# Optimization experiments

Hardware: AMD Instinct MI355X
Metric: run time of the kernel (lower is better)

Reference implementation:

```python
import jax, jax.numpy as jnp
import numpy as np

EPS = 1e-8

def _safe_norm(x):
    # L2 norm over last axis with zero (not NaN) gradient at x == 0,
    # matching torch.norm's subgradient convention.
    sq = jnp.sum(x * x, axis=-1, keepdims=True)
    nz = sq > 0
    return jnp.sqrt(jnp.where(nz, sq, 1.0)) * jnp.where(nz, 1.0, 0.0)

def _dihedral(p1, p2, p3, p4):
    # p*: [..., 3] -> angle [...], signed, in radians
    v1 = p2 - p1
    v2 = p3 - p2
    v3 = p4 - p3
    n1 = jnp.cross(v1, v2)
    n2 = jnp.cross(v2, v3)
    n1n = n1 / (_safe_norm(n1) + EPS)
    n2n = n2 / (_safe_norm(n2) + EPS)
    cos_angle = jnp.clip(jnp.sum(n1n * n2n, axis=-1), -1.0, 1.0)
    angle = jnp.arccos(cos_angle)
    sign = jnp.sign(jnp.sum(n1n * v3, axis=-1))
    return angle * sign

def setup_inputs() -> dict:
    key = jax.random.key(0)
    k1, k2, k3 = jax.random.split(key, 3)
    B, L, D = 64, 4096, 64
    backbone_coords = jax.random.normal(k1, (B, L, 4, 3), dtype=jnp.float32)
    # nn.Linear(6, 64): kaiming-uniform-ish init, bound = 1/sqrt(6)
    bound = 1.0 / np.sqrt(6.0)
    W = jax.random.uniform(k2, (D, 6), minval=-bound, maxval=bound, dtype=jnp.float32)
    b = jax.random.uniform(k3, (D,), minval=-bound, maxval=bound, dtype=jnp.float32)
    return {"backbone_coords": backbone_coords, "W": W, "b": b}

def reference(backbone_coords, W, b):
    # backbone_coords: [B, L, 4, 3] with atoms N, CA, C, O
    N = backbone_coords[:, :, 0, :]
    CA = backbone_coords[:, :, 1, :]
    C = backbone_coords[:, :, 2, :]

    # Shifted neighbors, duplicating boundary atoms exactly as the loop branches do.
    C_prev = jnp.concatenate([C[:, :1], C[:, :-1]], axis=1)      # phi i==0: p1 = C[0]
    N_next = jnp.concatenate([N[:, 1:], N[:, -1:]], axis=1)      # psi i==L-1: p4 = N[L-1]
    om_p3 = jnp.concatenate([N[:, 1:], CA[:, -1:]], axis=1)      # omega i==L-1: p3 = CA[L-1]
    om_p4 = jnp.concatenate([CA[:, 1:], CA[:, -1:]], axis=1)     # omega i==L-1: p4 = CA[L-1]

    phi = _dihedral(C_prev, N, CA, C)     # [B, L]
    psi = _dihedral(N, CA, C, N_next)     # [B, L]
    omega = _dihedral(CA, C, om_p3, om_p4)  # [B, L]

    angles = jnp.stack([phi, psi, omega], axis=-1)                     # [B, L, 3]
    encoded = jnp.concatenate([jnp.sin(angles), jnp.cos(angles)], axis=-1)  # [B, L, 6]
    return encoded @ W.T + b              # [B, L, 64]
```

## Files before the change

kernel.cpp:

```cpp
#include <hip/hip_runtime.h>

#define L_RES 4096
#define EPSF 1e-8f

struct V3 { float x, y, z; };

__device__ __forceinline__ V3 v3sub(V3 a, V3 b) { return {a.x-b.x, a.y-b.y, a.z-b.z}; }
__device__ __forceinline__ V3 v3cross(V3 a, V3 b) {
    return {a.y*b.z - a.z*b.y, a.z*b.x - a.x*b.z, a.x*b.y - a.y*b.x};
}
__device__ __forceinline__ float v3dot(V3 a, V3 b) { return a.x*b.x + a.y*b.y + a.z*b.z; }

__device__ __forceinline__ void dihedral_sc(V3 p1, V3 p2, V3 p3, V3 p4,
                                            float& s_out, float& c_out) {
    V3 v1 = v3sub(p2, p1);
    V3 v2 = v3sub(p3, p2);
    V3 v3 = v3sub(p4, p3);
    V3 n1 = v3cross(v1, v2);
    V3 n2 = v3cross(v2, v3);
    float sq1 = v3dot(n1, n1);
    float sq2 = v3dot(n2, n2);
    float nrm1 = (sq1 > 0.f) ? sqrtf(sq1) : 0.f;
    float nrm2 = (sq2 > 0.f) ? sqrtf(sq2) : 0.f;
    float inv1 = 1.f / (nrm1 + EPSF);
    float inv2 = 1.f / (nrm2 + EPSF);
    float c = (n1.x*n2.x + n1.y*n2.y + n1.z*n2.z) * (inv1 * inv2);
    c = fminf(1.f, fmaxf(-1.f, c));
    float sg = (n1.x*v3.x + n1.y*v3.y + n1.z*v3.z) * inv1;
    float sgn = (sg > 0.f) ? 1.f : ((sg < 0.f) ? -1.f : 0.f);
    float s = sqrtf(fmaxf(0.f, (1.f - c) * (1.f + c)));
    s_out = sgn * s;
    c_out = (sg == 0.f) ? 1.f : c;
}

__global__ __launch_bounds__(256) void dihedral_enc_kernel(
        const float* __restrict__ coords,
        const float* __restrict__ W,
        const float* __restrict__ bias,
        float* __restrict__ out) {
    __shared__ float enc_s[256 * 7];

    const int t   = threadIdx.x;
    const int blk = blockIdx.x;
    const int b   = blk >> 4;
    const int l   = ((blk & 15) << 8) + t;

    const long rowf = (long)b * L_RES * 12;
    const long ownf = rowf + (long)l * 12;
    const float4* c4 = (const float4*)coords;

    float4 a0 = c4[(ownf >> 2) + 0];
    float4 a1 = c4[(ownf >> 2) + 1];
    float  a2x = coords[ownf + 8];
    V3 N  = {a0.x, a0.y, a0.z};
    V3 CA = {a0.w, a1.x, a1.y};
    V3 C  = {a1.z, a1.w, a2x};

    const int lp = (l == 0) ? 0 : (l - 1);
    const long pf = rowf + (long)lp * 12;
    float4 pv = c4[(pf >> 2) + 1];
    float  p8 = coords[pf + 8];
    V3 C_prev = {pv.z, pv.w, p8};

    const bool is_last = (l == L_RES - 1);
    const int ln = is_last ? l : (l + 1);
    const long nf = rowf + (long)ln * 12;
    float4 q0 = c4[(nf >> 2) + 0];
    float4 q1 = c4[(nf >> 2) + 1];
    V3 N_next  = {q0.x, q0.y, q0.z};
    V3 CA_next = {q0.w, q1.x, q1.y};

    V3 om3 = is_last ? CA : N_next;
    V3 om4 = is_last ? CA : CA_next;

    float s_phi, c_phi, s_psi, c_psi, s_om, c_om;
    dihedral_sc(C_prev, N, CA, C,      s_phi, c_phi);
    dihedral_sc(N, CA, C, N_next,      s_psi, c_psi);
    dihedral_sc(CA, C, om3, om4,       s_om,  c_om);

    float* e = &enc_s[t * 7];
    e[0] = s_phi; e[1] = s_psi; e[2] = s_om;
    e[3] = c_phi; e[4] = c_psi; e[5] = c_om;

    __syncthreads();

    const int d4 = (t & 15) << 2;
    float w[4][6], bb[4];
    #pragma unroll
    for (int j = 0; j < 4; ++j) {
        bb[j] = bias[d4 + j];
        #pragma unroll
        for (int k = 0; k < 6; ++k) w[j][k] = W[(d4 + j) * 6 + k];
    }

    const int rg = t >> 4;
    float4* outp = (float4*)out;
    const long ob4 = (long)blk * 4096;
    #pragma unroll 4
    for (int it = 0; it < 16; ++it) {
        const int r = it * 16 + rg;
        const float* er = &enc_s[r * 7];
        float e0 = er[0], e1 = er[1], e2 = er[2];
        float e3 = er[3], e4 = er[4], e5 = er[5];
        float4 o;
        o.x = fmaf(e0, w[0][0], fmaf(e1, w[0][1], fmaf(e2, w[0][2],
              fmaf(e3, w[0][3], fmaf(e4, w[0][4], fmaf(e5, w[0][5], bb[0]))))));
        o.y = fmaf(e0, w[1][0], fmaf(e1, w[1][1], fmaf(e2, w[1][2],
              fmaf(e3, w[1][3], fmaf(e4, w[1][4], fmaf(e5, w[1][5], bb[1]))))));
        o.z = fmaf(e0, w[2][0], fmaf(e1, w[2][1], fmaf(e2, w[2][2],
              fmaf(e3, w[2][3], fmaf(e4, w[2][4], fmaf(e5, w[2][5], bb[2]))))));
        o.w = fmaf(e0, w[3][0], fmaf(e1, w[3][1], fmaf(e2, w[3][2],
              fmaf(e3, w[3][3], fmaf(e4, w[3][4], fmaf(e5, w[3][5], bb[3]))))));
        outp[ob4 + it * 256 + t] = o;
    }
}

extern "C" void kernel_launch(void* const* d_in, const int* in_sizes, int n_in,
                              void* d_out, int out_size, void* d_ws, size_t ws_size,
                              hipStream_t stream) {
    const float* coords = (const float*)d_in[0];
    const float* W      = (const float*)d_in[1];
    const float* bias   = (const float*)d_in[2];
    float* out          = (float*)d_out;

    const int total_res = in_sizes[0] / 12;
    const int blocks    = total_res / 256;
    dihedral_enc_kernel<<<blocks, 256, 0, stream>>>(coords, W, bias, out);
}
```

Baseline: 83.32 us.

## Split dihedrals across threads, shrink residues per block, use nontemporal stores

Each block now handles 64 residues instead of 256. Three groups of 64 threads each compute one dihedral type (phi, psi, omega), and the fourth wavefront idles during that phase. This cuts per-thread serial math and register pressure and quadruples the block count. Output writes use nontemporal stores so the 64 MB output stream bypasses cache. The cost is an idle wave during the angle phase and some redundant coordinate loads across the threads that share a residue.

```diff
diff --git a/kernel.cpp b/kernel.cpp
--- a/kernel.cpp
+++ b/kernel.cpp
@@ -2,6 +2,9 @@
 
 #define L_RES 4096
 #define EPSF 1e-8f
+#define RPB 64
+
+typedef float floatx4 __attribute__((ext_vector_type(4)));
 
 struct V3 { float x, y, z; };
 
@@ -38,51 +41,12 @@
         const float* __restrict__ W,
         const float* __restrict__ bias,
         float* __restrict__ out) {
-    __shared__ float enc_s[256 * 7];
+    __shared__ float enc_s[RPB * 7];
 
     const int t   = threadIdx.x;
     const int blk = blockIdx.x;
-    const int b   = blk >> 4;
-    const int l   = ((blk & 15) << 8) + t;
-
-    const long rowf = (long)b * L_RES * 12;
-    const long ownf = rowf + (long)l * 12;
-    const float4* c4 = (const float4*)coords;
-
-    float4 a0 = c4[(ownf >> 2) + 0];
-    float4 a1 = c4[(ownf >> 2) + 1];
-    float  a2x = coords[ownf + 8];
-    V3 N  = {a0.x, a0.y, a0.z};
-    V3 CA = {a0.w, a1.x, a1.y};
-    V3 C  = {a1.z, a1.w, a2x};
-
-    const int lp = (l == 0) ? 0 : (l - 1);
-    const long pf = rowf + (long)lp * 12;
-    float4 pv = c4[(pf >> 2) + 1];
-    float  p8 = coords[pf + 8];
-    V3 C_prev = {pv.z, pv.w, p8};
-
-    const bool is_last = (l == L_RES - 1);
-    const int ln = is_last ? l : (l + 1);
-    const long nf = rowf + (long)ln * 12;
-    float4 q0 = c4[(nf >> 2) + 0];
-    float4 q1 = c4[(nf >> 2) + 1];
-    V3 N_next  = {q0.x, q0.y, q0.z};
-    V3 CA_next = {q0.w, q1.x, q1.y};
-
-    V3 om3 = is_last ? CA : N_next;
-    V3 om4 = is_last ? CA : CA_next;
-
-    float s_phi, c_phi, s_psi, c_psi, s_om, c_om;
-    dihedral_sc(C_prev, N, CA, C,      s_phi, c_phi);
-    dihedral_sc(N, CA, C, N_next,      s_psi, c_psi);
-    dihedral_sc(CA, C, om3, om4,       s_om,  c_om);
-
-    float* e = &enc_s[t * 7];
-    e[0] = s_phi; e[1] = s_psi; e[2] = s_om;
-    e[3] = c_phi; e[4] = c_psi; e[5] = c_om;
-
-    __syncthreads();
+    const int b   = blk >> 6;
+    const int l0  = (blk & 63) << 6;
 
     const int d4 = (t & 15) << 2;
     float w[4][6], bb[4];
@@ -93,16 +57,62 @@
         for (int k = 0; k < 6; ++k) w[j][k] = W[(d4 + j) * 6 + k];
     }
 
+    const long rowf = (long)b * L_RES * 12;
+    const float4* c4 = (const float4*)coords;
+
+    const int d = t >> 6;
+    const int r = t & 63;
+    const int l = l0 + r;
+
+    if (d < 3) {
+        const long ownf = rowf + (long)l * 12;
+        float4 a0 = c4[(ownf >> 2) + 0];
+        float4 a1 = c4[(ownf >> 2) + 1];
+        float  a2x = coords[ownf + 8];
+        V3 N  = {a0.x, a0.y, a0.z};
+        V3 CA = {a0.w, a1.x, a1.y};
+        V3 C  = {a1.z, a1.w, a2x};
+
+        float s, c;
+        if (d == 0) {
+            const int lp = (l == 0) ? 0 : (l - 1);
+            const long pf = rowf + (long)lp * 12;
+            float4 pv = c4[(pf >> 2) + 1];
+            float  p8 = coords[pf + 8];
+            V3 C_prev = {pv.z, pv.w, p8};
+            dihedral_sc(C_prev, N, CA, C, s, c);
+        } else if (d == 1) {
+            const int ln = (l == L_RES - 1) ? l : (l + 1);
+            const long nf = rowf + (long)ln * 12;
+            float4 q0 = c4[(nf >> 2) + 0];
+            V3 N_next = {q0.x, q0.y, q0.z};
+            dihedral_sc(N, CA, C, N_next, s, c);
+        } else {
+            const bool is_last = (l == L_RES - 1);
+            const int ln = is_last ? l : (l + 1);
+            const long nf = rowf + (long)ln * 12;
+            float4 q0 = c4[(nf >> 2) + 0];
+            float4 q1 = c4[(nf >> 2) + 1];
+            V3 om3 = is_last ? CA : V3{q0.x, q0.y, q0.z};
+            V3 om4 = is_last ? CA : V3{q0.w, q1.x, q1.y};
+            dihedral_sc(CA, C, om3, om4, s, c);
+        }
+        enc_s[r * 7 + d]     = s;
+        enc_s[r * 7 + 3 + d] = c;
+    }
+
+    __syncthreads();
+
     const int rg = t >> 4;
-    float4* outp = (float4*)out;
-    const long ob4 = (long)blk * 4096;
-    #pragma unroll 4
-    for (int it = 0; it < 16; ++it) {
-        const int r = it * 16 + rg;
-        const float* er = &enc_s[r * 7];
+    floatx4* outp = (floatx4*)out;
+    const long ob4 = (long)blk * (RPB * 16);
+    #pragma unroll
+    for (int it = 0; it < 4; ++it) {
+        const int rr = it * 16 + rg;
+        const float* er = &enc_s[rr * 7];
         float e0 = er[0], e1 = er[1], e2 = er[2];
         float e3 = er[3], e4 = er[4], e5 = er[5];
-        float4 o;
+        floatx4 o;
         o.x = fmaf(e0, w[0][0], fmaf(e1, w[0][1], fmaf(e2, w[0][2],
               fmaf(e3, w[0][3], fmaf(e4, w[0][4], fmaf(e5, w[0][5], bb[0]))))));
         o.y = fmaf(e0, w[1][0], fmaf(e1, w[1][1], fmaf(e2, w[1][2],
@@ -111,7 +121,7 @@
               fmaf(e3, w[2][3], fmaf(e4, w[2][4], fmaf(e5, w[2][5], bb[2]))))));
         o.w = fmaf(e0, w[3][0], fmaf(e1, w[3][1], fmaf(e2, w[3][2],
               fmaf(e3, w[3][3], fmaf(e4, w[3][4], fmaf(e5, w[3][5], bb[3]))))));
-        outp[ob4 + it * 256 + t] = o;
+        __builtin_nontemporal_store(o, &outp[ob4 + it * 256 + t]);
     }
 }
 
@@ -124,6 +134,6 @@
     float* out          = (float*)d_out;
 
     const int total_res = in_sizes[0] / 12;
-    const int blocks    = total_res / 256;
+    const int blocks    = total_res / RPB;
     dihedral_enc_kernel<<<blocks, 256, 0, stream>>>(coords, W, bias, out);
 }
```

After: 87.03 us. +4.5%, slower.

## Stage residue coordinates in shared memory with halo and use nontemporal output stores

Applied to the files above, without the earlier changes.

Each block now loads its 256 residues plus one halo residue on each side into shared memory once. Neighbor C_prev, N_next and CA_next are then read from LDS instead of issuing redundant global loads per thread. The W/bias register loads are moved before the barrier, and output stores become nontemporal to avoid polluting cache with the large write-only output. This adds a barrier and LDS traffic, and the 9-float stride may cause bank conflicts.

```diff
diff --git a/kernel.cpp b/kernel.cpp
--- a/kernel.cpp
+++ b/kernel.cpp
@@ -2,6 +2,8 @@
 
 #define L_RES 4096
 #define EPSF 1e-8f
+
+typedef float floatx4 __attribute__((ext_vector_type(4)));
 
 struct V3 { float x, y, z; };
 
@@ -38,51 +40,52 @@
         const float* __restrict__ W,
         const float* __restrict__ bias,
         float* __restrict__ out) {
+    __shared__ float crd[258 * 9];
     __shared__ float enc_s[256 * 7];
 
     const int t   = threadIdx.x;
     const int blk = blockIdx.x;
     const int b   = blk >> 4;
-    const int l   = ((blk & 15) << 8) + t;
+    const int l0  = (blk & 15) << 8;
 
     const long rowf = (long)b * L_RES * 12;
-    const long ownf = rowf + (long)l * 12;
     const float4* c4 = (const float4*)coords;
 
-    float4 a0 = c4[(ownf >> 2) + 0];
-    float4 a1 = c4[(ownf >> 2) + 1];
-    float  a2x = coords[ownf + 8];
-    V3 N  = {a0.x, a0.y, a0.z};
-    V3 CA = {a0.w, a1.x, a1.y};
-    V3 C  = {a1.z, a1.w, a2x};
+    for (int j = t; j < 258; j += 256) {
+        int lc = l0 - 1 + j;
+        lc = (lc < 0) ? 0 : ((lc >= L_RES) ? (L_RES - 1) : lc);
+        const long f = rowf + (long)lc * 12;
+        float4 a0 = c4[(f >> 2) + 0];
+        float4 a1 = c4[(f >> 2) + 1];
+        float  a8 = coords[f + 8];
+        float* e = &crd[j * 9];
+        e[0] = a0.x; e[1] = a0.y; e[2] = a0.z; e[3] = a0.w;
+        e[4] = a1.x; e[5] = a1.y; e[6] = a1.z; e[7] = a1.w;
+        e[8] = a8;
+    }
+    __syncthreads();
 
-    const int lp = (l == 0) ? 0 : (l - 1);
-    const long pf = rowf + (long)lp * 12;
-    float4 pv = c4[(pf >> 2) + 1];
-    float  p8 = coords[pf + 8];
-    V3 C_prev = {pv.z, pv.w, p8};
-
+    const int l = l0 + t;
+    const float* ep = &crd[t * 9];
+    const float* eo = &crd[(t + 1) * 9];
+    const float* en = &crd[(t + 2) * 9];
+    V3 C_prev = {ep[6], ep[7], ep[8]};
+    V3 N      = {eo[0], eo[1], eo[2]};
+    V3 CA     = {eo[3], eo[4], eo[5]};
+    V3 C      = {eo[6], eo[7], eo[8]};
+    V3 N_next = {en[0], en[1], en[2]};
     const bool is_last = (l == L_RES - 1);
-    const int ln = is_last ? l : (l + 1);
-    const long nf = rowf + (long)ln * 12;
-    float4 q0 = c4[(nf >> 2) + 0];
-    float4 q1 = c4[(nf >> 2) + 1];
-    V3 N_next  = {q0.x, q0.y, q0.z};
-    V3 CA_next = {q0.w, q1.x, q1.y};
-
     V3 om3 = is_last ? CA : N_next;
-    V3 om4 = is_last ? CA : CA_next;
+    V3 om4 = is_last ? CA : V3{en[3], en[4], en[5]};
 
     float s_phi, c_phi, s_psi, c_psi, s_om, c_om;
-    dihedral_sc(C_prev, N, CA, C,      s_phi, c_phi);
-    dihedral_sc(N, CA, C, N_next,      s_psi, c_psi);
-    dihedral_sc(CA, C, om3, om4,       s_om,  c_om);
+    dihedral_sc(C_prev, N, CA, C,  s_phi, c_phi);
+    dihedral_sc(N, CA, C, N_next,  s_psi, c_psi);
+    dihedral_sc(CA, C, om3, om4,   s_om,  c_om);
 
     float* e = &enc_s[t * 7];
     e[0] = s_phi; e[1] = s_psi; e[2] = s_om;
     e[3] = c_phi; e[4] = c_psi; e[5] = c_om;
-
-    __syncthreads();
 
     const int d4 = (t & 15) << 2;
     float w[4][6], bb[4];
@@ -93,16 +96,18 @@
         for (int k = 0; k < 6; ++k) w[j][k] = W[(d4 + j) * 6 + k];
     }
 
+    __syncthreads();
+
     const int rg = t >> 4;
-    float4* outp = (float4*)out;
+    floatx4* outp = (floatx4*)out;
     const long ob4 = (long)blk * 4096;
     #pragma unroll 4
     for (int it = 0; it < 16; ++it) {
-        const int r = it * 16 + rg;
-        const float* er = &enc_s[r * 7];
+        const int rr = it * 16 + rg;
+        const float* er = &enc_s[rr * 7];
         float e0 = er[0], e1 = er[1], e2 = er[2];
         float e3 = er[3], e4 = er[4], e5 = er[5];
-        float4 o;
+        floatx4 o;
         o.x = fmaf(e0, w[0][0], fmaf(e1, w[0][1], fmaf(e2, w[0][2],
               fmaf(e3, w[0][3], fmaf(e4, w[0][4], fmaf(e5, w[0][5], bb[0]))))));
         o.y = fmaf(e0, w[1][0], fmaf(e1, w[1][1], fmaf(e2, w[1][2],
@@ -111,7 +116,7 @@
               fmaf(e3, w[2][3], fmaf(e4, w[2][4], fmaf(e5, w[2][5], bb[2]))))));
         o.w = fmaf(e0, w[3][0], fmaf(e1, w[3][1], fmaf(e2, w[3][2],
               fmaf(e3, w[3][3], fmaf(e4, w[3][4], fmaf(e5, w[3][5], bb[3]))))));
-        outp[ob4 + it * 256 + t] = o;
+        __builtin_nontemporal_store(o, &outp[ob4 + it * 256 + t]);
     }
 }
 
```

New measurement: 85.45 us. 1.03x slower.
